# Kernel tuning notes

Hardware: AMD Instinct MI355X
Metric: run time of the kernel (lower is better)

Reference implementation:

```python
import jax, jax.numpy as jnp
import numpy as np

EPS = 1e-12  # F.normalize clamp eps
LOGIT_SCALE = float(np.exp(np.log(100.0)))  # coattn_logit_scale.exp() == 100.0


def _l2norm(x):
    n = jnp.linalg.norm(x, axis=-1, keepdims=True)
    return x / jnp.maximum(n, EPS)


def setup_inputs() -> dict:
    key = jax.random.key(0)
    k1, k2, k3, k4 = jax.random.split(key, 4)
    B, N, C = 1, 100000, 1024
    NUM_QUERY = 10  # +1 gated query
    X = jax.random.normal(k1, (B, N, C), dtype=jnp.float32)
    Q = jax.random.normal(k2, (NUM_QUERY + 1, C), dtype=jnp.float32)
    W = jax.random.normal(k3, (C, C), dtype=jnp.float32) * (1.0 / np.sqrt(C))
    b = jax.random.normal(k4, (C,), dtype=jnp.float32) * 0.01
    return {"X": X, "Q": Q, "W": W, "b": b}


def reference(X, Q, W, b):
    # X: [1, N, C] bag features; Q: [num_query+1, C]; W,b: visual_adapter Linear
    Qn = _l2norm(Q)[None]            # [1, q+1, C]
    Xn = _l2norm(X)                  # [1, N, C]
    A_ = jnp.einsum('bqc,bnc->bqn', Qn, Xn)   # cosine similarities [1, q+1, N]
    # gated-query subtraction: last query's scores subtracted from the rest
    A_ = A_[:, :-1, :] - A_[:, -1:, :]        # [1, q, N]
    A = jax.nn.softmax(LOGIT_SCALE * A_, axis=-1)
    out = jnp.einsum('bqn,bnc->bqc', A, X)    # [1, q, C]
    pooled = jnp.mean(out, axis=1)            # 'mean' query pooling -> [1, C]
    return pooled @ W.T + b                   # visual_adapter (nn.Linear)
```

## Files before the change

kernel.cpp:

```cpp
#include <hip/hip_runtime.h>
#include <float.h>
#include <math.h>

#define C    1024
#define NQ   10
#define G4   500
#define LGS  16
#define RSUB 25

template <int CTRL, int ROWM>
__device__ __forceinline__ float dpp_add(float x) {
  int mv = __builtin_amdgcn_update_dpp(0, __float_as_int(x), CTRL, ROWM, 0xf, true);
  return x + __int_as_float(mv);
}
__device__ __forceinline__ float wave_sum64(float x) {
  x = dpp_add<0xB1,  0xf>(x);
  x = dpp_add<0x4E,  0xf>(x);
  x = dpp_add<0x141, 0xf>(x);
  x = dpp_add<0x140, 0xf>(x);
  x = dpp_add<0x142, 0xa>(x);
  x = dpp_add<0x143, 0xc>(x);
  return __int_as_float(__builtin_amdgcn_readlane(__float_as_int(x), 63));
}

__global__ __launch_bounds__(256) void k0_qdiff(const float* __restrict__ Q,
                                                float* __restrict__ qd) {
  __shared__ float red[256];
  __shared__ float inorm[NQ + 1];
  int t = threadIdx.x;
  for (int k = 0; k <= NQ; ++k) {
    float s = 0.f;
    for (int c = t; c < C; c += 256) { float v = Q[k * C + c]; s = fmaf(v, v, s); }
    red[t] = s; __syncthreads();
    for (int st = 128; st > 0; st >>= 1) {
      if (t < st) red[t] += red[t + st];
      __syncthreads();
    }
    if (t == 0) inorm[k] = 1.0f / fmaxf(sqrtf(red[0]), 1e-12f);
    __syncthreads();
  }
  for (int k = 0; k < NQ; ++k)
    for (int c = t; c < C; c += 256)
      qd[k * C + c] = Q[k * C + c] * inorm[k] - Q[NQ * C + c] * inorm[NQ];
}

__global__ __launch_bounds__(256, 2) void kf_fused(const float* __restrict__ X,
                                                   const float* __restrict__ qd,
                                                   float* __restrict__ partial,
                                                   float* __restrict__ dsum,
                                                   float* __restrict__ mblk,
                                                   int N, int rpb) {
  __shared__ float lgbuf[2][RSUB][LGS];
  __shared__ float wmS[4][8];
  __shared__ float sMnew[16];

  const int g = blockIdx.x, t = threadIdx.x;
  const int l = t & 63, wv = t >> 6;
  const int pr = wv >> 1;
  const int qbase = (wv & 1) * 5;
  const int co = l << 2;

  const int n0 = g * rpb;
  const int n1 = min(n0 + rpb, N);

  float4 q4[5][4];
#pragma unroll
  for (int k = 0; k < 5; ++k)
#pragma unroll
    for (int j = 0; j < 4; ++j)
      q4[k][j] = *(const float4*)(qd + (qbase + k) * C + j * 256 + co);

  float a[NQ][4], ds[NQ], mo[NQ];
#pragma unroll
  for (int k = 0; k < NQ; ++k) {
    a[k][0] = a[k][1] = a[k][2] = a[k][3] = 0.f;
    ds[k] = 0.f; mo[k] = -FLT_MAX;
  }

  int s = 0;
  for (int c0 = n0; c0 < n1; c0 += RSUB) {
    const int cnt = min(RSUB, n1 - c0);

    float wmx[5];
#pragma unroll
    for (int k = 0; k < 5; ++k) wmx[k] = -FLT_MAX;

    for (int i = pr; i < cnt; i += 2) {
      const float* xp = X + (size_t)(c0 + i) * C + co;
      float4 xv[4];
#pragma unroll
      for (int j = 0; j < 4; ++j) xv[j] = *(const float4*)(xp + j * 256);

      float ss = 0.f, dot[5];
#pragma unroll
      for (int k = 0; k < 5; ++k) dot[k] = 0.f;
#pragma unroll
      for (int j = 0; j < 4; ++j) {
        float4 v = xv[j];
        ss = fmaf(v.x, v.x, fmaf(v.y, v.y, fmaf(v.z, v.z, fmaf(v.w, v.w, ss))));
#pragma unroll
        for (int k = 0; k < 5; ++k) {
          float4 q = q4[k][j];
          dot[k] = fmaf(v.x, q.x, fmaf(v.y, q.y, fmaf(v.z, q.z, fmaf(v.w, q.w, dot[k]))));
        }
      }
      float ssu = wave_sum64(ss);
      float rn  = 100.0f / fmaxf(sqrtf(ssu), 1e-12f);
#pragma unroll
      for (int k = 0; k < 5; ++k) {
        float lg = wave_sum64(dot[k]) * rn;
        wmx[k] = fmaxf(wmx[k], lg);
        if (l == 0) lgbuf[s][i][qbase + k] = lg;
      }
    }
    if (l == 0) {
#pragma unroll
      for (int k = 0; k < 5; ++k) wmS[wv][k] = wmx[k];
    }
    __syncthreads();

#pragma unroll
    for (int k = 0; k < NQ; ++k) {
      float cm = (k < 5) ? fmaxf(wmS[0][k], wmS[2][k])
                         : fmaxf(wmS[1][k - 5], wmS[3][k - 5]);
      float mn = fmaxf(mo[k], cm);
      float sc = __expf(mo[k] - mn);
      ds[k] *= sc;
      a[k][0] *= sc; a[k][1] *= sc; a[k][2] *= sc; a[k][3] *= sc;
      mo[k] = mn;
      if (t == 0) sMnew[k] = mn;
    }
    __syncthreads();

    for (int idx = t; idx < cnt * LGS; idx += 256) {
      int rr = idx >> 4, k = idx & 15;
      if (k < NQ) lgbuf[s][rr][k] = __expf(lgbuf[s][rr][k] - sMnew[k]);
    }
    __syncthreads();

#pragma unroll 2
    for (int i = 0; i < cnt; ++i) {
      float4 x4 = *(const float4*)&X[(size_t)(c0 + i) * C + (t << 2)];
      float4 wA = *(const float4*)&lgbuf[s][i][0];
      float4 wB = *(const float4*)&lgbuf[s][i][4];
      float2 wC = *(const float2*)&lgbuf[s][i][8];
#define ACC(K, W)                                            \
      ds[K] += (W);                                          \
      a[K][0] = fmaf((W), x4.x, a[K][0]);                    \
      a[K][1] = fmaf((W), x4.y, a[K][1]);                    \
      a[K][2] = fmaf((W), x4.z, a[K][2]);                    \
      a[K][3] = fmaf((W), x4.w, a[K][3]);
      ACC(0, wA.x) ACC(1, wA.y) ACC(2, wA.z) ACC(3, wA.w)
      ACC(4, wB.x) ACC(5, wB.y) ACC(6, wB.z) ACC(7, wB.w)
      ACC(8, wC.x) ACC(9, wC.y)
#undef ACC
    }
    s ^= 1;
  }

#pragma unroll
  for (int k = 0; k < NQ; ++k) {
    float4 o; o.x = a[k][0]; o.y = a[k][1]; o.z = a[k][2]; o.w = a[k][3];
    *(float4*)&partial[(((size_t)(g * NQ + k)) << 10) + (t << 2)] = o;
  }
  if (t == 0) {
#pragma unroll
    for (int k = 0; k < NQ; ++k) {
      dsum[g * NQ + k] = ds[k];
      mblk[g * 16 + k] = mo[k];
    }
  }
}

__global__ __launch_bounds__(256) void k5a_pooled(const float* __restrict__ partial,
                                                  const float* __restrict__ dsum,
                                                  const float* __restrict__ mblk,
                                                  float* __restrict__ pooled) {
  __shared__ float sM[16], sF[16];
  __shared__ float red[256];
  __shared__ float r4[256][4];
  int t = threadIdx.x;
  int k = t & 15, grp = t >> 4;

  float mm = -FLT_MAX;
  if (k < NQ)
    for (int g = grp; g < G4; g += 16) mm = fmaxf(mm, mblk[g * 16 + k]);
  red[t] = mm; __syncthreads();
  if (t < 16) {
    float m2 = red[t];
    for (int j = 1; j < 16; ++j) m2 = fmaxf(m2, red[t + 16 * j]);
    sM[t] = m2;
  }
  __syncthreads();

  float dd = 0.f;
  if (k < NQ) {
    float Mk = sM[k];
    for (int g = grp; g < G4; g += 16)
      dd += dsum[g * NQ + k] * __expf(mblk[g * 16 + k] - Mk);
  }
  red[t] = dd; __syncthreads();
  if (t < 16) {
    float d2 = 0.f;
    for (int j = 0; j < 16; ++j) d2 += red[t + 16 * j];
    sF[t] = 1.0f / ((float)NQ * d2);
  }
  __syncthreads();

  int c0 = blockIdx.x * 4;
  float a0 = 0.f, a1 = 0.f, a2 = 0.f, a3 = 0.f;
  for (int idx = t; idx < G4 * NQ; idx += 256) {
    int g = idx / NQ, kq = idx - g * NQ;
    float f = __expf(mblk[g * 16 + kq] - sM[kq]) * sF[kq];
    const float4 p = *(const float4*)&partial[(((size_t)idx) << 10) + c0];
    a0 = fmaf(p.x, f, a0); a1 = fmaf(p.y, f, a1);
    a2 = fmaf(p.z, f, a2); a3 = fmaf(p.w, f, a3);
  }
  r4[t][0] = a0; r4[t][1] = a1; r4[t][2] = a2; r4[t][3] = a3;
  __syncthreads();
  for (int st = 128; st > 0; st >>= 1) {
    if (t < st) {
      r4[t][0] += r4[t + st][0]; r4[t][1] += r4[t + st][1];
      r4[t][2] += r4[t + st][2]; r4[t][3] += r4[t + st][3];
    }
    __syncthreads();
  }
  if (t < 4) pooled[c0 + t] = r4[0][t];
}

__global__ __launch_bounds__(256) void k5b_out(const float* __restrict__ W,
                                               const float* __restrict__ bias,
                                               const float* __restrict__ pooled,
                                               float* __restrict__ out) {
  __shared__ float sp[C];
  int t = threadIdx.x;
  for (int i = t; i < C; i += 256) sp[i] = pooled[i];
  __syncthreads();
  int wv = t >> 6, lane = t & 63;
#pragma unroll
  for (int jj = 0; jj < 8; ++jj) {
    int j = blockIdx.x * 32 + wv * 8 + jj;
    float s = 0.f;
#pragma unroll
    for (int seg = 0; seg < 4; ++seg) {
      int cbase = seg * 256 + lane * 4;
      float4 w4 = *(const float4*)&W[(size_t)j * C + cbase];
      float4 p4 = *(const float4*)&sp[cbase];
      s += w4.x * p4.x + w4.y * p4.y + w4.z * p4.z + w4.w * p4.w;
    }
#pragma unroll
    for (int off = 32; off > 0; off >>= 1) s += __shfl_down(s, off);
    if (lane == 0) out[j] = s + bias[j];
  }
}

extern "C" void kernel_launch(void* const* d_in, const int* in_sizes, int n_in,
                              void* d_out, int out_size, void* d_ws, size_t ws_size,
                              hipStream_t stream) {
  const float* X = (const float*)d_in[0];
  const float* Q = (const float*)d_in[1];
  const float* W = (const float*)d_in[2];
  const float* b = (const float*)d_in[3];
  float* out = (float*)d_out;

  int N   = in_sizes[0] / C;
  int rpb = (N + G4 - 1) / G4;

  float* ws      = (float*)d_ws;
  float* qd      = ws;
  float* mblk    = qd + NQ * C;
  float* dsum    = mblk + G4 * 16;
  float* pooled  = dsum + G4 * NQ;
  float* partial = pooled + C;

  hipLaunchKernelGGL(k0_qdiff,  dim3(1),      dim3(256), 0, stream, Q, qd);
  hipLaunchKernelGGL(kf_fused,  dim3(G4),     dim3(256), 0, stream,
                     X, qd, partial, dsum, mblk, N, rpb);
  hipLaunchKernelGGL(k5a_pooled,dim3(C / 4),  dim3(256), 0, stream,
                     partial, dsum, mblk, pooled);
  hipLaunchKernelGGL(k5b_out,   dim3(C / 32), dim3(256), 0, stream, W, b, pooled, out);
}
```

Measured before the change: 696.8 us.

## Fuse logits and weighted accumulation into a single-pass online softmax per wave

Each wave pair now streams its own rows with a strided assignment. It computes logits and immediately applies an online-softmax rescale and accumulation, so X is read once instead of twice. Loads are double-buffered in registers, and the per-chunk shared-memory logit buffers and block barriers are removed. The two row-halves are merged at the end through a 40KB shared buffer. This trades extra per-row exp and conditional-rescale work and more register pressure for less memory traffic and synchronisation.

```diff
diff --git a/kernel.cpp b/kernel.cpp
--- a/kernel.cpp
+++ b/kernel.cpp
@@ -2,11 +2,10 @@
 #include <float.h>
 #include <math.h>
 
-#define C    1024
-#define NQ   10
-#define G4   500
-#define LGS  16
-#define RSUB 25
+#define C     1024
+#define NQ    10
+#define G4    512
+#define NPAIR (G4 * 2)
 
 template <int CTRL, int ROWM>
 __device__ __forceinline__ float dpp_add(float x) {
@@ -21,6 +20,14 @@
   x = dpp_add<0x142, 0xa>(x);
   x = dpp_add<0x143, 0xc>(x);
   return __int_as_float(__builtin_amdgcn_readlane(__float_as_int(x), 63));
+}
+
+__device__ __forceinline__ void scale4(float4& v, float s) {
+  v.x *= s; v.y *= s; v.z *= s; v.w *= s;
+}
+__device__ __forceinline__ void fma4(float4& acc, float w, const float4& x) {
+  acc.x = fmaf(w, x.x, acc.x); acc.y = fmaf(w, x.y, acc.y);
+  acc.z = fmaf(w, x.z, acc.z); acc.w = fmaf(w, x.w, acc.w);
 }
 
 __global__ __launch_bounds__(256) void k0_qdiff(const float* __restrict__ Q,
@@ -49,19 +56,13 @@
                                                    float* __restrict__ partial,
                                                    float* __restrict__ dsum,
                                                    float* __restrict__ mblk,
-                                                   int N, int rpb) {
-  __shared__ float lgbuf[2][RSUB][LGS];
-  __shared__ float wmS[4][8];
-  __shared__ float sMnew[16];
-
-  const int g = blockIdx.x, t = threadIdx.x;
+                                                   int N) {
+  const int t = threadIdx.x;
   const int l = t & 63, wv = t >> 6;
   const int pr = wv >> 1;
   const int qbase = (wv & 1) * 5;
   const int co = l << 2;
-
-  const int n0 = g * rpb;
-  const int n1 = min(n0 + rpb, N);
+  const int pid = blockIdx.x * 2 + pr;
 
   float4 q4[5][4];
 #pragma unroll
@@ -70,105 +71,123 @@
     for (int j = 0; j < 4; ++j)
       q4[k][j] = *(const float4*)(qd + (qbase + k) * C + j * 256 + co);
 
-  float a[NQ][4], ds[NQ], mo[NQ];
-#pragma unroll
-  for (int k = 0; k < NQ; ++k) {
-    a[k][0] = a[k][1] = a[k][2] = a[k][3] = 0.f;
+  float4 a[5][4];
+  float ds[5], mo[5];
+#pragma unroll
+  for (int k = 0; k < 5; ++k) {
+    a[k][0] = a[k][1] = a[k][2] = a[k][3] = make_float4(0.f, 0.f, 0.f, 0.f);
     ds[k] = 0.f; mo[k] = -FLT_MAX;
   }
 
-  int s = 0;
-  for (int c0 = n0; c0 < n1; c0 += RSUB) {
-    const int cnt = min(RSUB, n1 - c0);
-
-    float wmx[5];
-#pragma unroll
-    for (int k = 0; k < 5; ++k) wmx[k] = -FLT_MAX;
-
-    for (int i = pr; i < cnt; i += 2) {
-      const float* xp = X + (size_t)(c0 + i) * C + co;
-      float4 xv[4];
-#pragma unroll
-      for (int j = 0; j < 4; ++j) xv[j] = *(const float4*)(xp + j * 256);
-
-      float ss = 0.f, dot[5];
-#pragma unroll
-      for (int k = 0; k < 5; ++k) dot[k] = 0.f;
+  auto loadrow = [&](float4* dst, int rr) {
+    const float* xp = X + (size_t)rr * C + co;
+    dst[0] = *(const float4*)(xp);
+    dst[1] = *(const float4*)(xp + 256);
+    dst[2] = *(const float4*)(xp + 512);
+    dst[3] = *(const float4*)(xp + 768);
+  };
+
+  auto proc = [&](const float4* xv) {
+    float ss = 0.f;
+    float dt[5];
+#pragma unroll
+    for (int k = 0; k < 5; ++k) dt[k] = 0.f;
+#pragma unroll
+    for (int j = 0; j < 4; ++j) {
+      float4 v = xv[j];
+      ss = fmaf(v.x, v.x, fmaf(v.y, v.y, fmaf(v.z, v.z, fmaf(v.w, v.w, ss))));
+#pragma unroll
+      for (int k = 0; k < 5; ++k) {
+        float4 q = q4[k][j];
+        dt[k] = fmaf(v.x, q.x, fmaf(v.y, q.y, fmaf(v.z, q.z, fmaf(v.w, q.w, dt[k]))));
+      }
+    }
+    float rn = 100.0f / fmaxf(sqrtf(wave_sum64(ss)), 1e-12f);
+#pragma unroll
+    for (int k = 0; k < 5; ++k) {
+      float lg = wave_sum64(dt[k]) * rn;
+      float mn = fmaxf(mo[k], lg);
+      if (mn > mo[k]) {
+        float sc = __expf(mo[k] - mn);
+        ds[k] *= sc;
+        scale4(a[k][0], sc); scale4(a[k][1], sc);
+        scale4(a[k][2], sc); scale4(a[k][3], sc);
+        mo[k] = mn;
+      }
+      float w = __expf(lg - mo[k]);
+      ds[k] += w;
+      fma4(a[k][0], w, xv[0]); fma4(a[k][1], w, xv[1]);
+      fma4(a[k][2], w, xv[2]); fma4(a[k][3], w, xv[3]);
+    }
+  };
+
+  {
+    float4 xa[4], xb[4];
+    int r = pid;
+    loadrow(xa, r);
+    int rn = r + NPAIR;
+    for (;;) {
+      if (rn < N) loadrow(xb, rn);
+      proc(xa);
+      if (rn >= N) break;
+      r = rn; rn = r + NPAIR;
+      if (rn < N) loadrow(xa, rn);
+      proc(xb);
+      if (rn >= N) break;
+      r = rn; rn = r + NPAIR;
+    }
+  }
+
+  __shared__ float wm[4][8];
+  __shared__ float wd[4][8];
+  __shared__ float part[NQ][C];
+  if (l == 0) {
+#pragma unroll
+    for (int k = 0; k < 5; ++k) { wm[wv][k] = mo[k]; wd[wv][k] = ds[k]; }
+  }
+  __syncthreads();
+  float sc[5];
+#pragma unroll
+  for (int k = 0; k < 5; ++k) {
+    float M = fmaxf(wm[wv][k], wm[wv ^ 2][k]);
+    sc[k] = __expf(mo[k] - M);
+  }
+  if (wv < 2) {
+#pragma unroll
+    for (int k = 0; k < 5; ++k)
 #pragma unroll
       for (int j = 0; j < 4; ++j) {
-        float4 v = xv[j];
-        ss = fmaf(v.x, v.x, fmaf(v.y, v.y, fmaf(v.z, v.z, fmaf(v.w, v.w, ss))));
-#pragma unroll
-        for (int k = 0; k < 5; ++k) {
-          float4 q = q4[k][j];
-          dot[k] = fmaf(v.x, q.x, fmaf(v.y, q.y, fmaf(v.z, q.z, fmaf(v.w, q.w, dot[k]))));
-        }
+        float4 o = a[k][j]; scale4(o, sc[k]);
+        *(float4*)&part[qbase + k][j * 256 + co] = o;
       }
-      float ssu = wave_sum64(ss);
-      float rn  = 100.0f / fmaxf(sqrtf(ssu), 1e-12f);
-#pragma unroll
-      for (int k = 0; k < 5; ++k) {
-        float lg = wave_sum64(dot[k]) * rn;
-        wmx[k] = fmaxf(wmx[k], lg);
-        if (l == 0) lgbuf[s][i][qbase + k] = lg;
+  }
+  __syncthreads();
+  if (wv >= 2) {
+#pragma unroll
+    for (int k = 0; k < 5; ++k)
+#pragma unroll
+      for (int j = 0; j < 4; ++j) {
+        float4 p = *(const float4*)&part[qbase + k][j * 256 + co];
+        float4 o = a[k][j];
+        p.x = fmaf(o.x, sc[k], p.x); p.y = fmaf(o.y, sc[k], p.y);
+        p.z = fmaf(o.z, sc[k], p.z); p.w = fmaf(o.w, sc[k], p.w);
+        *(float4*)&part[qbase + k][j * 256 + co] = p;
       }
-    }
-    if (l == 0) {
-#pragma unroll
-      for (int k = 0; k < 5; ++k) wmS[wv][k] = wmx[k];
-    }
-    __syncthreads();
-
-#pragma unroll
-    for (int k = 0; k < NQ; ++k) {
-      float cm = (k < 5) ? fmaxf(wmS[0][k], wmS[2][k])
-                         : fmaxf(wmS[1][k - 5], wmS[3][k - 5]);
-      float mn = fmaxf(mo[k], cm);
-      float sc = __expf(mo[k] - mn);
-      ds[k] *= sc;
-      a[k][0] *= sc; a[k][1] *= sc; a[k][2] *= sc; a[k][3] *= sc;
-      mo[k] = mn;
-      if (t == 0) sMnew[k] = mn;
-    }
-    __syncthreads();
-
-    for (int idx = t; idx < cnt * LGS; idx += 256) {
-      int rr = idx >> 4, k = idx & 15;
-      if (k < NQ) lgbuf[s][rr][k] = __expf(lgbuf[s][rr][k] - sMnew[k]);
-    }
-    __syncthreads();
-
-#pragma unroll 2
-    for (int i = 0; i < cnt; ++i) {
-      float4 x4 = *(const float4*)&X[(size_t)(c0 + i) * C + (t << 2)];
-      float4 wA = *(const float4*)&lgbuf[s][i][0];
-      float4 wB = *(const float4*)&lgbuf[s][i][4];
-      float2 wC = *(const float2*)&lgbuf[s][i][8];
-#define ACC(K, W)                                            \
-      ds[K] += (W);                                          \
-      a[K][0] = fmaf((W), x4.x, a[K][0]);                    \
-      a[K][1] = fmaf((W), x4.y, a[K][1]);                    \
-      a[K][2] = fmaf((W), x4.z, a[K][2]);                    \
-      a[K][3] = fmaf((W), x4.w, a[K][3]);
-      ACC(0, wA.x) ACC(1, wA.y) ACC(2, wA.z) ACC(3, wA.w)
-      ACC(4, wB.x) ACC(5, wB.y) ACC(6, wB.z) ACC(7, wB.w)
-      ACC(8, wC.x) ACC(9, wC.y)
-#undef ACC
-    }
-    s ^= 1;
-  }
-
-#pragma unroll
-  for (int k = 0; k < NQ; ++k) {
-    float4 o; o.x = a[k][0]; o.y = a[k][1]; o.z = a[k][2]; o.w = a[k][3];
-    *(float4*)&partial[(((size_t)(g * NQ + k)) << 10) + (t << 2)] = o;
-  }
-  if (t == 0) {
-#pragma unroll
-    for (int k = 0; k < NQ; ++k) {
-      dsum[g * NQ + k] = ds[k];
-      mblk[g * 16 + k] = mo[k];
-    }
+  }
+  __syncthreads();
+
+  {
+    const float4* src = (const float4*)&part[0][0];
+    float4* dst = (float4*)&partial[(size_t)blockIdx.x * NQ * C];
+    for (int idx = t; idx < NQ * (C / 4); idx += 256) dst[idx] = src[idx];
+  }
+  if (t < NQ) {
+    int w0 = (t < 5) ? 0 : 1, k5 = (t < 5) ? t : t - 5;
+    float m0 = wm[w0][k5], m1 = wm[w0 + 2][k5];
+    float M = fmaxf(m0, m1);
+    dsum[blockIdx.x * NQ + t] =
+        wd[w0][k5] * __expf(m0 - M) + wd[w0 + 2][k5] * __expf(m1 - M);
+    mblk[blockIdx.x * 16 + t] = M;
   }
 }
 
@@ -263,8 +282,7 @@
   const float* b = (const float*)d_in[3];
   float* out = (float*)d_out;
 
-  int N   = in_sizes[0] / C;
-  int rpb = (N + G4 - 1) / G4;
+  int N = in_sizes[0] / C;
 
   float* ws      = (float*)d_ws;
   float* qd      = ws;
@@ -275,7 +293,7 @@
 
   hipLaunchKernelGGL(k0_qdiff,  dim3(1),      dim3(256), 0, stream, Q, qd);
   hipLaunchKernelGGL(kf_fused,  dim3(G4),     dim3(256), 0, stream,
-                     X, qd, partial, dsum, mblk, N, rpb);
+                     X, qd, partial, dsum, mblk, N);
   hipLaunchKernelGGL(k5a_pooled,dim3(C / 4),  dim3(256), 0, stream,
                      partial, dsum, mblk, pooled);
   hipLaunchKernelGGL(k5b_out,   dim3(C / 32), dim3(256), 0, stream, W, b, pooled, out);
```

New measurement: 1.101 ms. 58.0% more time.
